# Optimization experiments

Measured on AMD Instinct MI355X. Metric: run time of the kernel, lower is better.

The kernel has to match this reference:

```python
import jax, jax.numpy as jnp
import numpy as np

B, LX, LM, D = 4, 512, 512, 256

def setup_inputs() -> dict:
    key = jax.random.key(0)
    ks = jax.random.split(key, 7)
    s = 1.0 / np.sqrt(D)
    return {
        "x": jax.random.normal(ks[0], (B, LX, D), jnp.float32),
        "memory": jax.random.normal(ks[1], (B, LM, D), jnp.float32),
        "memory_mask": jax.random.randint(ks[2], (B, LM), 0, 2, jnp.int32),
        "W1": jax.random.normal(ks[3], (D, D), jnp.float32) * s,
        "b1": jax.random.normal(ks[4], (D,), jnp.float32) * s,
        "W2": jax.random.normal(ks[5], (D, D), jnp.float32) * s,
        "Wt": jax.random.normal(ks[6], (D,), jnp.float32) * s,
    }

def reference(x, memory, memory_mask, W1, b1, W2, Wt):
    # item1: (B, Lx, D); item2: (B, Lm, D)
    item1 = jnp.einsum("bxd,ed->bxe", x, W1) + b1
    item2 = jnp.einsum("bmd,ed->bme", memory, W2)
    # additive attention: tanh of broadcast sum, then reduce D to scalar logit
    item = item1[:, :, None, :] + item2[:, None, :, :]  # (B, Lx, Lm, D)
    S_logit = jnp.einsum("bxmd,d->bxm", jnp.tanh(item), Wt)
    S_logit = jnp.where(memory_mask[:, None, :] == 0, jnp.float32(-10000.0), S_logit)
    return S_logit
```

## Files before the change

### kernel.cpp

```cpp
#include <hip/hip_runtime.h>

namespace {

constexpr int B = 4, LX = 512, LM = 512, D = 256;
constexpr float KSCALE = 2.8853900817779268f;
constexpr float CLAMP = 7.5f;

typedef __attribute__((ext_vector_type(8))) short short8;
typedef __attribute__((ext_vector_type(4))) float f32x4;
typedef __attribute__((ext_vector_type(2))) float f32x2;

__device__ __forceinline__ unsigned bfbits(float f) {
    unsigned u = __float_as_uint(f);
    u += 0x7FFFu + ((u >> 16) & 1u);
    return u >> 16;
}
__device__ __forceinline__ int pack2(float a, float b) {
    return (int)(bfbits(a) | (bfbits(b) << 16));
}
__device__ __forceinline__ f32x2 up2r(unsigned u) {
    f32x2 r;
    r.x = __uint_as_float(u << 16);
    r.y = __uint_as_float(u);
    return r;
}
__device__ __forceinline__ unsigned permb(unsigned hi, unsigned lo, unsigned sel) {
    return __builtin_amdgcn_perm(hi, lo, sel);
}

__global__ __launch_bounds__(256) void proj_mfma(
    const float* __restrict__ x, const float* __restrict__ mem,
    const float* __restrict__ W1, const float* __restrict__ b1v,
    const float* __restrict__ W2,
    unsigned short* __restrict__ E1h, unsigned short* __restrict__ E2h)
{
    const int tid = threadIdx.x;
    const int m0c = blockIdx.x * 32;
    const int e0  = blockIdx.y * 64;
    const int z   = m0c >= 2048;
    const int r0  = z ? (m0c - 2048) : m0c;
    const float* __restrict__ A = (z ? mem : x) + (size_t)r0 * D;
    const float* __restrict__ W = z ? W2 : W1;

    __shared__ short sA[8][32][40];
    __shared__ short sW[8][64][40];

    const int wid = tid >> 6, lane = tid & 63;
    const int lr = lane & 15, quad = lane >> 4;
    const int g   = wid & 1;
    const int cg0 = (wid >> 1) * 2;
    const int srA = tid >> 3;
    const int scA = (tid & 7) * 4;

#pragma unroll
    for (int kc8 = 0; kc8 < 8; ++kc8) {
        const int kc = kc8 * 32;
        const float4 av = *(const float4*)&A[(size_t)srA * D + kc + scA];
        const float4 w0 = *(const float4*)&W[(size_t)(e0 + srA) * D + kc + scA];
        const float4 w1 = *(const float4*)&W[(size_t)(e0 + 32 + srA) * D + kc + scA];
        *(int2*)&sA[kc8][srA][scA]      = make_int2(pack2(av.x, av.y), pack2(av.z, av.w));
        *(int2*)&sW[kc8][srA][scA]      = make_int2(pack2(w0.x, w0.y), pack2(w0.z, w0.w));
        *(int2*)&sW[kc8][srA + 32][scA] = make_int2(pack2(w1.x, w1.y), pack2(w1.z, w1.w));
    }
    __syncthreads();

    f32x4 acc0 = {0.f, 0.f, 0.f, 0.f};
    f32x4 acc1 = {0.f, 0.f, 0.f, 0.f};
#pragma unroll
    for (int kc8 = 0; kc8 < 8; ++kc8) {
        short8 af  = *(const short8*)&sA[kc8][g * 16 + lr][quad * 8];
        short8 bf0 = *(const short8*)&sW[kc8][cg0 * 16 + lr][quad * 8];
        short8 bf1 = *(const short8*)&sW[kc8][cg0 * 16 + 16 + lr][quad * 8];
        acc0 = __builtin_amdgcn_mfma_f32_16x16x32_bf16(af, bf0, acc0, 0, 0, 0);
        acc1 = __builtin_amdgcn_mfma_f32_16x16x32_bf16(af, bf1, acc1, 0, 0, 0);
    }

    const float bias0 = z ? 0.f : b1v[e0 + cg0 * 16 + lr];
    const float bias1 = z ? 0.f : b1v[e0 + cg0 * 16 + 16 + lr];
    const int ec0 = e0 + cg0 * 16 + lr;
#pragma unroll
    for (int reg = 0; reg < 4; ++reg) {
        const int pair = quad * 4 + reg;
        float a0 = KSCALE * (acc0[reg] + bias0);
        float a1 = KSCALE * (acc1[reg] + bias1);
        a0 = fminf(fmaxf(a0, -CLAMP), CLAMP);
        a1 = fminf(fmaxf(a1, -CLAMP), CLAMP);
        const unsigned short e0b = (unsigned short)bfbits(__builtin_amdgcn_exp2f(a0));
        const unsigned short e1b = (unsigned short)bfbits(__builtin_amdgcn_exp2f(a1));
        if (!z) {
            const size_t base = (size_t)((r0 >> 5) * 16 + pair) * 256;
            E1h[(base + ec0) * 2 + g]      = e0b;
            E1h[(base + ec0 + 16) * 2 + g] = e1b;
        } else {
            const int row = r0 + g * 16 + pair;
            E2h[(size_t)row * 256 + ec0]      = e0b;
            E2h[(size_t)row * 256 + ec0 + 16] = e1b;
        }
    }
}

constexpr int RS = 268;
constexpr int C1 = 136;

__global__ __launch_bounds__(256, 4) void tanh_score_kernel(
    const unsigned* __restrict__ E1p, const unsigned* __restrict__ E2u,
    const float* __restrict__ Wt, const int* __restrict__ mask,
    float* __restrict__ out)
{
    const int tid = threadIdx.x;
    const int b   = blockIdx.z;
    const int yb  = blockIdx.y;
    const int T   = yb >> 1;
    const int p0  = (yb & 1) * 8;
    const int bx  = blockIdx.x;

    __shared__ unsigned sA[8 * RS];
    __shared__ unsigned sB[16 * RS];
    __shared__ int scid[LM];
    __shared__ int smsk[LM];
    __shared__ float4 sRed[128];

    const int lane = tid & 63;
    const int wid  = tid >> 6;

    int mvv[8];
#pragma unroll
    for (int c = 0; c < 8; ++c) mvv[c] = mask[b * LM + c * 64 + lane];
    int count = 0, mcount = 0;
#pragma unroll
    for (int c = 0; c < 8; ++c) {
        const bool bit = mvv[c] != 0;
        const unsigned long long bal = __ballot(bit);
        const unsigned long long lt  = (1ull << lane) - 1ull;
        const int pre  = __popcll(bal & lt);
        const int prem = __popcll(~bal & lt);
        if (wid == 0) {
            if (bit) scid[count + pre]   = c * 64 + lane;
            else     smsk[mcount + prem] = c * 64 + lane;
        }
        const int pc = __popcll(bal);
        count  += pc;
        mcount += 64 - pc;
    }

    {
        const int rA = tid >> 5, q2 = tid & 31;
        const unsigned* g =
            E1p + (size_t)((b * 16 + T) * 16 + p0 + rA) * 256 + q2 * 8;
        const int off = rA * RS + q2 * 8 + (q2 >= 16 ? 8 : 0);
        *(uint4*)&sA[off]     = *(const uint4*)(g);
        *(uint4*)&sA[off + 4] = *(const uint4*)(g + 4);
    }

    float sumW = 0.f;
#pragma unroll
    for (int i = 0; i < 256; i += 4) {
        const float4 w = *(const float4*)&Wt[i];
        sumW += (w.x + w.y) + (w.z + w.w);
    }

    __syncthreads();

    const int tx = tid & 15;
    const int ty = (tid >> 4) & 7;
    const int h  = tid >> 7;
    const int hb = h * 128;
    const int ho = h * C1;
    const f32x2 one2 = {1.f, 1.f};

#define SPL(s)  ((f32x2){(s), (s)})
#define FMA2(A_, B_, C_) __builtin_elementwise_fma((A_), (B_), (C_))
#define OCT(BX, accv) { \
    const f32x2 T0 = FMA2(a_[0], BX(0), one2), T1 = FMA2(a_[1], BX(1), one2); \
    const f32x2 T2 = FMA2(a_[2], BX(2), one2), T3 = FMA2(a_[3], BX(3), one2); \
    const f32x2 T4 = FMA2(a_[4], BX(4), one2), T5 = FMA2(a_[5], BX(5), one2); \
    const f32x2 T6 = FMA2(a_[6], BX(6), one2), T7 = FMA2(a_[7], BX(7), one2); \
    const f32x2 L0 = T0 * T1, L1 = T2 * T3, L2 = T4 * T5, L3 = T6 * T7;       \
    const f32x2 Q0 = L0 * L1, Q1 = L2 * L3;                                   \
    const f32x2 den = Q0 * Q1;                                                \
    const f32x2 n0 = FMA2(SPL(wv[0]), T1, SPL(wv[1]) * T0);                   \
    const f32x2 n1 = FMA2(SPL(wv[2]), T3, SPL(wv[3]) * T2);                   \
    const f32x2 n2 = FMA2(SPL(wv[4]), T5, SPL(wv[5]) * T4);                   \
    const f32x2 n3 = FMA2(SPL(wv[6]), T7, SPL(wv[7]) * T6);                   \
    const f32x2 u0 = FMA2(n0, L1, n1 * L0), u1 = FMA2(n2, L3, n3 * L2);       \
    const f32x2 N  = FMA2(u0, Q1, u1 * Q0);                                   \
    f32x2 r; r.x = __builtin_amdgcn_rcpf(den.x);                              \
             r.y = __builtin_amdgcn_rcpf(den.y);                              \
    (accv) = FMA2(N, r, (accv)); }
#define BP(i)  (p_[i])
#define BPS(i) (__builtin_shufflevector(p_[i], p_[i], 1, 0))

    for (int s = bx; s < 16; s += 8) {
        const int m0 = s * 32;
        if (m0 >= count) break;

        {
            const int rB = tid >> 4, q = tid & 15;
            const int clo = min(m0 + rB, count - 1);
            const int chi = min(m0 + rB + 16, count - 1);
            const unsigned* rlo = E2u + (size_t)(b * LM + scid[clo]) * 128 + q * 8;
            const unsigned* rhi = E2u + (size_t)(b * LM + scid[chi]) * 128 + q * 8;
            const uint4 Lo0 = *(const uint4*)(rlo);
            const uint4 Lo1 = *(const uint4*)(rlo + 4);
            const uint4 Hi0 = *(const uint4*)(rhi);
            const uint4 Hi1 = *(const uint4*)(rhi + 4);
            const int ob = rB * RS + q * 16 + (q >= 8 ? 8 : 0);
            uint4 P;
            P.x = permb(Hi0.x, Lo0.x, 0x05040100u); P.y = permb(Hi0.x, Lo0.x, 0x07060302u);
            P.z = permb(Hi0.y, Lo0.y, 0x05040100u); P.w = permb(Hi0.y, Lo0.y, 0x07060302u);
            *(uint4*)&sB[ob] = P;
            P.x = permb(Hi0.z, Lo0.z, 0x05040100u); P.y = permb(Hi0.z, Lo0.z, 0x07060302u);
            P.z = permb(Hi0.w, Lo0.w, 0x05040100u); P.w = permb(Hi0.w, Lo0.w, 0x07060302u);
            *(uint4*)&sB[ob + 4] = P;
            P.x = permb(Hi1.x, Lo1.x, 0x05040100u); P.y = permb(Hi1.x, Lo1.x, 0x07060302u);
            P.z = permb(Hi1.y, Lo1.y, 0x05040100u); P.w = permb(Hi1.y, Lo1.y, 0x07060302u);
            *(uint4*)&sB[ob + 8] = P;
            P.x = permb(Hi1.z, Lo1.z, 0x05040100u); P.y = permb(Hi1.z, Lo1.z, 0x07060302u);
            P.z = permb(Hi1.w, Lo1.w, 0x05040100u); P.w = permb(Hi1.w, Lo1.w, 0x07060302u);
            *(uint4*)&sB[ob + 12] = P;
        }
        __syncthreads();

        f32x2 accs = {0.f, 0.f}, accw = {0.f, 0.f};
#pragma unroll 1
        for (int d = 0; d < 128; d += 8) {
            const uint4 ua0 = *(const uint4*)&sA[ty * RS + ho + d];
            const uint4 ua1 = *(const uint4*)&sA[ty * RS + ho + d + 4];
            const uint4 ub0 = *(const uint4*)&sB[tx * RS + ho + d];
            const uint4 ub1 = *(const uint4*)&sB[tx * RS + ho + d + 4];
            const float4 w0 = *(const float4*)&Wt[hb + d];
            const float4 w1 = *(const float4*)&Wt[hb + d + 4];

            const f32x2 a_[8] = {up2r(ua0.x), up2r(ua0.y), up2r(ua0.z), up2r(ua0.w),
                                 up2r(ua1.x), up2r(ua1.y), up2r(ua1.z), up2r(ua1.w)};
            const f32x2 p_[8] = {up2r(ub0.x), up2r(ub0.y), up2r(ub0.z), up2r(ub0.w),
                                 up2r(ub1.x), up2r(ub1.y), up2r(ub1.z), up2r(ub1.w)};
            const float wv[8] = {w0.x, w0.y, w0.z, w0.w, w1.x, w1.y, w1.z, w1.w};

            OCT(BP,  accs)
            OCT(BPS, accw)
        }

        if (h) sRed[ty * 16 + tx] = make_float4(accs.x, accs.y, accw.x, accw.y);
        __syncthreads();
        if (!h) {
            const float4 r = sRed[ty * 16 + tx];
            const int xA = T * 32 + p0 + ty, xB = xA + 16;
            const int col0 = m0 + tx, col1 = m0 + 16 + tx;
            if (col0 < count) {
                const int mo = scid[col0];
                out[((size_t)b * LX + xA) * LM + mo] = sumW - 2.f * (accs.x + r.x);
                out[((size_t)b * LX + xB) * LM + mo] = sumW - 2.f * (accw.y + r.w);
            }
            if (col1 < count) {
                const int mo = scid[col1];
                out[((size_t)b * LX + xA) * LM + mo] = sumW - 2.f * (accw.x + r.z);
                out[((size_t)b * LX + xB) * LM + mo] = sumW - 2.f * (accs.y + r.y);
            }
        }
    }
#undef BP
#undef BPS
#undef OCT
#undef FMA2
#undef SPL

    if (bx == 0) {
        const int xA = T * 32 + p0 + ty, xB = xA + 16;
        const int idx = h * 16 + tx;
        for (int k = idx; k < mcount; k += 32) {
            const int mo = smsk[k];
            out[((size_t)b * LX + xA) * LM + mo] = -10000.f;
            out[((size_t)b * LX + xB) * LM + mo] = -10000.f;
        }
    }
}

}

extern "C" void kernel_launch(void* const* d_in, const int* in_sizes, int n_in,
                              void* d_out, int out_size, void* d_ws, size_t ws_size,
                              hipStream_t stream)
{
    const float* x    = (const float*)d_in[0];
    const float* mem  = (const float*)d_in[1];
    const int*   mask = (const int*)d_in[2];
    const float* W1   = (const float*)d_in[3];
    const float* b1   = (const float*)d_in[4];
    const float* W2   = (const float*)d_in[5];
    const float* Wt   = (const float*)d_in[6];
    float* out = (float*)d_out;

    unsigned*       E1p = (unsigned*)d_ws;
    unsigned short* E2h = (unsigned short*)(E1p + (size_t)(B * LX / 32) * 16 * 256);

    proj_mfma<<<dim3(128, 4), 256, 0, stream>>>(
        x, mem, W1, b1, W2, (unsigned short*)E1p, E2h);

    tanh_score_kernel<<<dim3(8, 32, 4), 256, 0, stream>>>(
        E1p, (const unsigned*)E2h, Wt, mask, out);
}
```

Measured before the change: 96.92 us.

## Fuse projection and tanh-score kernels into one cooperative launch with grid sync

Merges the bf16 MFMA projection and the tanh-score kernel into a single persistent cooperative kernel of 1024 blocks. A grid-wide sync separates the phases, and a shared-memory union lets both phases reuse the same LDS. Projection tiles are re-split to 32x32 per block so the 1024 blocks cover both phases. The change also replaces the serial Wt sum with a wave shuffle reduction. It aims to remove the second launch and the gap between kernels, at the cost of a grid barrier and a need for 4 resident blocks per CU, with the two-kernel path kept as a fallback.

```diff
diff --git a/kernel.cpp b/kernel.cpp
--- a/kernel.cpp
+++ b/kernel.cpp
@@ -1,4 +1,7 @@
 #include <hip/hip_runtime.h>
+#include <hip/hip_cooperative_groups.h>
+
+namespace cg = cooperative_groups;
 
 namespace {
 
@@ -28,145 +31,8 @@
     return __builtin_amdgcn_perm(hi, lo, sel);
 }
 
-__global__ __launch_bounds__(256) void proj_mfma(
-    const float* __restrict__ x, const float* __restrict__ mem,
-    const float* __restrict__ W1, const float* __restrict__ b1v,
-    const float* __restrict__ W2,
-    unsigned short* __restrict__ E1h, unsigned short* __restrict__ E2h)
-{
-    const int tid = threadIdx.x;
-    const int m0c = blockIdx.x * 32;
-    const int e0  = blockIdx.y * 64;
-    const int z   = m0c >= 2048;
-    const int r0  = z ? (m0c - 2048) : m0c;
-    const float* __restrict__ A = (z ? mem : x) + (size_t)r0 * D;
-    const float* __restrict__ W = z ? W2 : W1;
-
-    __shared__ short sA[8][32][40];
-    __shared__ short sW[8][64][40];
-
-    const int wid = tid >> 6, lane = tid & 63;
-    const int lr = lane & 15, quad = lane >> 4;
-    const int g   = wid & 1;
-    const int cg0 = (wid >> 1) * 2;
-    const int srA = tid >> 3;
-    const int scA = (tid & 7) * 4;
-
-#pragma unroll
-    for (int kc8 = 0; kc8 < 8; ++kc8) {
-        const int kc = kc8 * 32;
-        const float4 av = *(const float4*)&A[(size_t)srA * D + kc + scA];
-        const float4 w0 = *(const float4*)&W[(size_t)(e0 + srA) * D + kc + scA];
-        const float4 w1 = *(const float4*)&W[(size_t)(e0 + 32 + srA) * D + kc + scA];
-        *(int2*)&sA[kc8][srA][scA]      = make_int2(pack2(av.x, av.y), pack2(av.z, av.w));
-        *(int2*)&sW[kc8][srA][scA]      = make_int2(pack2(w0.x, w0.y), pack2(w0.z, w0.w));
-        *(int2*)&sW[kc8][srA + 32][scA] = make_int2(pack2(w1.x, w1.y), pack2(w1.z, w1.w));
-    }
-    __syncthreads();
-
-    f32x4 acc0 = {0.f, 0.f, 0.f, 0.f};
-    f32x4 acc1 = {0.f, 0.f, 0.f, 0.f};
-#pragma unroll
-    for (int kc8 = 0; kc8 < 8; ++kc8) {
-        short8 af  = *(const short8*)&sA[kc8][g * 16 + lr][quad * 8];
-        short8 bf0 = *(const short8*)&sW[kc8][cg0 * 16 + lr][quad * 8];
-        short8 bf1 = *(const short8*)&sW[kc8][cg0 * 16 + 16 + lr][quad * 8];
-        acc0 = __builtin_amdgcn_mfma_f32_16x16x32_bf16(af, bf0, acc0, 0, 0, 0);
-        acc1 = __builtin_amdgcn_mfma_f32_16x16x32_bf16(af, bf1, acc1, 0, 0, 0);
-    }
-
-    const float bias0 = z ? 0.f : b1v[e0 + cg0 * 16 + lr];
-    const float bias1 = z ? 0.f : b1v[e0 + cg0 * 16 + 16 + lr];
-    const int ec0 = e0 + cg0 * 16 + lr;
-#pragma unroll
-    for (int reg = 0; reg < 4; ++reg) {
-        const int pair = quad * 4 + reg;
-        float a0 = KSCALE * (acc0[reg] + bias0);
-        float a1 = KSCALE * (acc1[reg] + bias1);
-        a0 = fminf(fmaxf(a0, -CLAMP), CLAMP);
-        a1 = fminf(fmaxf(a1, -CLAMP), CLAMP);
-        const unsigned short e0b = (unsigned short)bfbits(__builtin_amdgcn_exp2f(a0));
-        const unsigned short e1b = (unsigned short)bfbits(__builtin_amdgcn_exp2f(a1));
-        if (!z) {
-            const size_t base = (size_t)((r0 >> 5) * 16 + pair) * 256;
-            E1h[(base + ec0) * 2 + g]      = e0b;
-            E1h[(base + ec0 + 16) * 2 + g] = e1b;
-        } else {
-            const int row = r0 + g * 16 + pair;
-            E2h[(size_t)row * 256 + ec0]      = e0b;
-            E2h[(size_t)row * 256 + ec0 + 16] = e1b;
-        }
-    }
-}
-
 constexpr int RS = 268;
 constexpr int C1 = 136;
-
-__global__ __launch_bounds__(256, 4) void tanh_score_kernel(
-    const unsigned* __restrict__ E1p, const unsigned* __restrict__ E2u,
-    const float* __restrict__ Wt, const int* __restrict__ mask,
-    float* __restrict__ out)
-{
-    const int tid = threadIdx.x;
-    const int b   = blockIdx.z;
-    const int yb  = blockIdx.y;
-    const int T   = yb >> 1;
-    const int p0  = (yb & 1) * 8;
-    const int bx  = blockIdx.x;
-
-    __shared__ unsigned sA[8 * RS];
-    __shared__ unsigned sB[16 * RS];
-    __shared__ int scid[LM];
-    __shared__ int smsk[LM];
-    __shared__ float4 sRed[128];
-
-    const int lane = tid & 63;
-    const int wid  = tid >> 6;
-
-    int mvv[8];
-#pragma unroll
-    for (int c = 0; c < 8; ++c) mvv[c] = mask[b * LM + c * 64 + lane];
-    int count = 0, mcount = 0;
-#pragma unroll
-    for (int c = 0; c < 8; ++c) {
-        const bool bit = mvv[c] != 0;
-        const unsigned long long bal = __ballot(bit);
-        const unsigned long long lt  = (1ull << lane) - 1ull;
-        const int pre  = __popcll(bal & lt);
-        const int prem = __popcll(~bal & lt);
-        if (wid == 0) {
-            if (bit) scid[count + pre]   = c * 64 + lane;
-            else     smsk[mcount + prem] = c * 64 + lane;
-        }
-        const int pc = __popcll(bal);
-        count  += pc;
-        mcount += 64 - pc;
-    }
-
-    {
-        const int rA = tid >> 5, q2 = tid & 31;
-        const unsigned* g =
-            E1p + (size_t)((b * 16 + T) * 16 + p0 + rA) * 256 + q2 * 8;
-        const int off = rA * RS + q2 * 8 + (q2 >= 16 ? 8 : 0);
-        *(uint4*)&sA[off]     = *(const uint4*)(g);
-        *(uint4*)&sA[off + 4] = *(const uint4*)(g + 4);
-    }
-
-    float sumW = 0.f;
-#pragma unroll
-    for (int i = 0; i < 256; i += 4) {
-        const float4 w = *(const float4*)&Wt[i];
-        sumW += (w.x + w.y) + (w.z + w.w);
-    }
-
-    __syncthreads();
-
-    const int tx = tid & 15;
-    const int ty = (tid >> 4) & 7;
-    const int h  = tid >> 7;
-    const int hb = h * 128;
-    const int ho = h * C1;
-    const f32x2 one2 = {1.f, 1.f};
 
 #define SPL(s)  ((f32x2){(s), (s)})
 #define FMA2(A_, B_, C_) __builtin_elementwise_fma((A_), (B_), (C_))
@@ -189,6 +55,357 @@
     (accv) = FMA2(N, r, (accv)); }
 #define BP(i)  (p_[i])
 #define BPS(i) (__builtin_shufflevector(p_[i], p_[i], 1, 0))
+
+__global__ __launch_bounds__(256, 4) void fused_attn(
+    const float* __restrict__ x, const float* __restrict__ mem,
+    const int* __restrict__ mask,
+    const float* __restrict__ W1, const float* __restrict__ b1v,
+    const float* __restrict__ W2, const float* __restrict__ Wt,
+    unsigned* __restrict__ E1p, unsigned short* __restrict__ E2h,
+    float* __restrict__ out)
+{
+    union ShU {
+        struct { unsigned A[32 * 132]; unsigned W[32 * 132]; } p;
+        struct { unsigned sA[8 * RS]; unsigned sB[16 * RS];
+                 int scid[LM]; int smsk[LM]; float4 sRed[128]; } t;
+    };
+    __shared__ ShU sh;
+
+    const int tid  = threadIdx.x;
+    const int lane = tid & 63;
+    const int wid  = tid >> 6;
+
+    {
+        const int u    = blockIdx.x;
+        const int tile = u >> 3;
+        const int e0   = (u & 7) * 32;
+        const int m0c  = tile * 32;
+        const int z    = m0c >= 2048;
+        const int r0   = z ? (m0c - 2048) : m0c;
+        const float* __restrict__ A = (z ? mem : x) + (size_t)r0 * D;
+        const float* __restrict__ W = z ? W2 : W1;
+
+        const int sr  = tid >> 3;
+        const int scf = (tid & 7) * 32;
+
+        float4 a4[8], w4[8];
+#pragma unroll
+        for (int j = 0; j < 8; ++j) {
+            a4[j] = *(const float4*)&A[(size_t)sr * D + scf + j * 4];
+            w4[j] = *(const float4*)&W[(size_t)(e0 + sr) * D + scf + j * 4];
+        }
+#pragma unroll
+        for (int j = 0; j < 4; ++j) {
+            uint4 P;
+            P.x = pack2(a4[2*j].x,   a4[2*j].y);
+            P.y = pack2(a4[2*j].z,   a4[2*j].w);
+            P.z = pack2(a4[2*j+1].x, a4[2*j+1].y);
+            P.w = pack2(a4[2*j+1].z, a4[2*j+1].w);
+            *(uint4*)&sh.p.A[sr * 132 + (scf >> 1) + j * 4] = P;
+            P.x = pack2(w4[2*j].x,   w4[2*j].y);
+            P.y = pack2(w4[2*j].z,   w4[2*j].w);
+            P.z = pack2(w4[2*j+1].x, w4[2*j+1].y);
+            P.w = pack2(w4[2*j+1].z, w4[2*j+1].w);
+            *(uint4*)&sh.p.W[sr * 132 + (scf >> 1) + j * 4] = P;
+        }
+        __syncthreads();
+
+        const int lr = lane & 15, quad = lane >> 4;
+        const int g = wid & 1, cgq = wid >> 1;
+        f32x4 acc = {0.f, 0.f, 0.f, 0.f};
+#pragma unroll
+        for (int k8 = 0; k8 < 8; ++k8) {
+            short8 af = *(const short8*)&sh.p.A[(g*16 + lr)*132 + k8*16 + quad*4];
+            short8 bf = *(const short8*)&sh.p.W[(cgq*16 + lr)*132 + k8*16 + quad*4];
+            acc = __builtin_amdgcn_mfma_f32_16x16x32_bf16(af, bf, acc, 0, 0, 0);
+        }
+
+        const int ec = e0 + cgq * 16 + lr;
+        const float bias = z ? 0.f : b1v[ec];
+#pragma unroll
+        for (int reg = 0; reg < 4; ++reg) {
+            const int pair = quad * 4 + reg;
+            float a0 = KSCALE * (acc[reg] + bias);
+            a0 = fminf(fmaxf(a0, -CLAMP), CLAMP);
+            const unsigned short eb =
+                (unsigned short)bfbits(__builtin_amdgcn_exp2f(a0));
+            if (!z) {
+                ((unsigned short*)E1p)
+                    [(((size_t)(r0 >> 5) * 16 + pair) * 256 + ec) * 2 + g] = eb;
+            } else {
+                E2h[(size_t)(r0 + g * 16 + pair) * 256 + ec] = eb;
+            }
+        }
+    }
+
+    cg::this_grid().sync();
+
+    const int b  = blockIdx.x >> 8;
+    const int yb = (blockIdx.x >> 3) & 31;
+    const int bx = blockIdx.x & 7;
+    const int T  = yb >> 1;
+    const int p0 = (yb & 1) * 8;
+
+    int mvv[8];
+#pragma unroll
+    for (int c = 0; c < 8; ++c) mvv[c] = mask[b * LM + c * 64 + lane];
+    int count = 0, mcount = 0;
+#pragma unroll
+    for (int c = 0; c < 8; ++c) {
+        const bool bit = mvv[c] != 0;
+        const unsigned long long bal = __ballot(bit);
+        const unsigned long long lt  = (1ull << lane) - 1ull;
+        const int pre  = __popcll(bal & lt);
+        const int prem = __popcll(~bal & lt);
+        if (wid == 0) {
+            if (bit) sh.t.scid[count + pre]   = c * 64 + lane;
+            else     sh.t.smsk[mcount + prem] = c * 64 + lane;
+        }
+        const int pc = __popcll(bal);
+        count  += pc;
+        mcount += 64 - pc;
+    }
+
+    {
+        const int rA = tid >> 5, q2 = tid & 31;
+        const unsigned* g_ =
+            E1p + (size_t)((b * 16 + T) * 16 + p0 + rA) * 256 + q2 * 8;
+        const int off = rA * RS + q2 * 8 + (q2 >= 16 ? 8 : 0);
+        *(uint4*)&sh.t.sA[off]     = *(const uint4*)(g_);
+        *(uint4*)&sh.t.sA[off + 4] = *(const uint4*)(g_ + 4);
+    }
+
+    const float4 wsv = *(const float4*)&Wt[lane * 4];
+    float sumW = (wsv.x + wsv.y) + (wsv.z + wsv.w);
+#pragma unroll
+    for (int off = 32; off >= 1; off >>= 1) sumW += __shfl_xor(sumW, off);
+
+    __syncthreads();
+
+    const int tx = tid & 15;
+    const int ty = (tid >> 4) & 7;
+    const int h  = tid >> 7;
+    const int hb = h * 128;
+    const int ho = h * C1;
+    const f32x2 one2 = {1.f, 1.f};
+
+    for (int s = bx; s < 16; s += 8) {
+        const int m0 = s * 32;
+        if (m0 >= count) break;
+
+        {
+            const int rB = tid >> 4, q = tid & 15;
+            const int clo = min(m0 + rB, count - 1);
+            const int chi = min(m0 + rB + 16, count - 1);
+            const unsigned* rlo =
+                (const unsigned*)E2h + (size_t)(b * LM + sh.t.scid[clo]) * 128 + q * 8;
+            const unsigned* rhi =
+                (const unsigned*)E2h + (size_t)(b * LM + sh.t.scid[chi]) * 128 + q * 8;
+            const uint4 Lo0 = *(const uint4*)(rlo);
+            const uint4 Lo1 = *(const uint4*)(rlo + 4);
+            const uint4 Hi0 = *(const uint4*)(rhi);
+            const uint4 Hi1 = *(const uint4*)(rhi + 4);
+            const int ob = rB * RS + q * 16 + (q >= 8 ? 8 : 0);
+            uint4 P;
+            P.x = permb(Hi0.x, Lo0.x, 0x05040100u); P.y = permb(Hi0.x, Lo0.x, 0x07060302u);
+            P.z = permb(Hi0.y, Lo0.y, 0x05040100u); P.w = permb(Hi0.y, Lo0.y, 0x07060302u);
+            *(uint4*)&sh.t.sB[ob] = P;
+            P.x = permb(Hi0.z, Lo0.z, 0x05040100u); P.y = permb(Hi0.z, Lo0.z, 0x07060302u);
+            P.z = permb(Hi0.w, Lo0.w, 0x05040100u); P.w = permb(Hi0.w, Lo0.w, 0x07060302u);
+            *(uint4*)&sh.t.sB[ob + 4] = P;
+            P.x = permb(Hi1.x, Lo1.x, 0x05040100u); P.y = permb(Hi1.x, Lo1.x, 0x07060302u);
+            P.z = permb(Hi1.y, Lo1.y, 0x05040100u); P.w = permb(Hi1.y, Lo1.y, 0x07060302u);
+            *(uint4*)&sh.t.sB[ob + 8] = P;
+            P.x = permb(Hi1.z, Lo1.z, 0x05040100u); P.y = permb(Hi1.z, Lo1.z, 0x07060302u);
+            P.z = permb(Hi1.w, Lo1.w, 0x05040100u); P.w = permb(Hi1.w, Lo1.w, 0x07060302u);
+            *(uint4*)&sh.t.sB[ob + 12] = P;
+        }
+        __syncthreads();
+
+        f32x2 accs = {0.f, 0.f}, accw = {0.f, 0.f};
+#pragma unroll 1
+        for (int d = 0; d < 128; d += 8) {
+            const uint4 ua0 = *(const uint4*)&sh.t.sA[ty * RS + ho + d];
+            const uint4 ua1 = *(const uint4*)&sh.t.sA[ty * RS + ho + d + 4];
+            const uint4 ub0 = *(const uint4*)&sh.t.sB[tx * RS + ho + d];
+            const uint4 ub1 = *(const uint4*)&sh.t.sB[tx * RS + ho + d + 4];
+            const float4 w0 = *(const float4*)&Wt[hb + d];
+            const float4 w1 = *(const float4*)&Wt[hb + d + 4];
+
+            const f32x2 a_[8] = {up2r(ua0.x), up2r(ua0.y), up2r(ua0.z), up2r(ua0.w),
+                                 up2r(ua1.x), up2r(ua1.y), up2r(ua1.z), up2r(ua1.w)};
+            const f32x2 p_[8] = {up2r(ub0.x), up2r(ub0.y), up2r(ub0.z), up2r(ub0.w),
+                                 up2r(ub1.x), up2r(ub1.y), up2r(ub1.z), up2r(ub1.w)};
+            const float wv[8] = {w0.x, w0.y, w0.z, w0.w, w1.x, w1.y, w1.z, w1.w};
+
+            OCT(BP,  accs)
+            OCT(BPS, accw)
+        }
+
+        if (h) sh.t.sRed[ty * 16 + tx] = make_float4(accs.x, accs.y, accw.x, accw.y);
+        __syncthreads();
+        if (!h) {
+            const float4 r = sh.t.sRed[ty * 16 + tx];
+            const int xA = T * 32 + p0 + ty, xB = xA + 16;
+            const int col0 = m0 + tx, col1 = m0 + 16 + tx;
+            if (col0 < count) {
+                const int mo = sh.t.scid[col0];
+                out[((size_t)b * LX + xA) * LM + mo] = sumW - 2.f * (accs.x + r.x);
+                out[((size_t)b * LX + xB) * LM + mo] = sumW - 2.f * (accw.y + r.w);
+            }
+            if (col1 < count) {
+                const int mo = sh.t.scid[col1];
+                out[((size_t)b * LX + xA) * LM + mo] = sumW - 2.f * (accw.x + r.z);
+                out[((size_t)b * LX + xB) * LM + mo] = sumW - 2.f * (accs.y + r.y);
+            }
+        }
+    }
+
+    if (bx == 0) {
+        const int xA = T * 32 + p0 + ty, xB = xA + 16;
+        const int idx = h * 16 + tx;
+        for (int k = idx; k < mcount; k += 32) {
+            const int mo = sh.t.smsk[k];
+            out[((size_t)b * LX + xA) * LM + mo] = -10000.f;
+            out[((size_t)b * LX + xB) * LM + mo] = -10000.f;
+        }
+    }
+}
+
+__global__ __launch_bounds__(256) void proj_mfma(
+    const float* __restrict__ x, const float* __restrict__ mem,
+    const float* __restrict__ W1, const float* __restrict__ b1v,
+    const float* __restrict__ W2,
+    unsigned short* __restrict__ E1h, unsigned short* __restrict__ E2h)
+{
+    const int tid = threadIdx.x;
+    const int m0c = blockIdx.x * 32;
+    const int e0  = blockIdx.y * 64;
+    const int z   = m0c >= 2048;
+    const int r0  = z ? (m0c - 2048) : m0c;
+    const float* __restrict__ A = (z ? mem : x) + (size_t)r0 * D;
+    const float* __restrict__ W = z ? W2 : W1;
+
+    __shared__ short sA[8][32][40];
+    __shared__ short sW[8][64][40];
+
+    const int wid = tid >> 6, lane = tid & 63;
+    const int lr = lane & 15, quad = lane >> 4;
+    const int g   = wid & 1;
+    const int cg0 = (wid >> 1) * 2;
+    const int srA = tid >> 3;
+    const int scA = (tid & 7) * 4;
+
+#pragma unroll
+    for (int kc8 = 0; kc8 < 8; ++kc8) {
+        const int kc = kc8 * 32;
+        const float4 av = *(const float4*)&A[(size_t)srA * D + kc + scA];
+        const float4 w0 = *(const float4*)&W[(size_t)(e0 + srA) * D + kc + scA];
+        const float4 w1 = *(const float4*)&W[(size_t)(e0 + 32 + srA) * D + kc + scA];
+        *(int2*)&sA[kc8][srA][scA]      = make_int2(pack2(av.x, av.y), pack2(av.z, av.w));
+        *(int2*)&sW[kc8][srA][scA]      = make_int2(pack2(w0.x, w0.y), pack2(w0.z, w0.w));
+        *(int2*)&sW[kc8][srA + 32][scA] = make_int2(pack2(w1.x, w1.y), pack2(w1.z, w1.w));
+    }
+    __syncthreads();
+
+    f32x4 acc0 = {0.f, 0.f, 0.f, 0.f};
+    f32x4 acc1 = {0.f, 0.f, 0.f, 0.f};
+#pragma unroll
+    for (int kc8 = 0; kc8 < 8; ++kc8) {
+        short8 af  = *(const short8*)&sA[kc8][g * 16 + lr][quad * 8];
+        short8 bf0 = *(const short8*)&sW[kc8][cg0 * 16 + lr][quad * 8];
+        short8 bf1 = *(const short8*)&sW[kc8][cg0 * 16 + 16 + lr][quad * 8];
+        acc0 = __builtin_amdgcn_mfma_f32_16x16x32_bf16(af, bf0, acc0, 0, 0, 0);
+        acc1 = __builtin_amdgcn_mfma_f32_16x16x32_bf16(af, bf1, acc1, 0, 0, 0);
+    }
+
+    const float bias0 = z ? 0.f : b1v[e0 + cg0 * 16 + lr];
+    const float bias1 = z ? 0.f : b1v[e0 + cg0 * 16 + 16 + lr];
+    const int ec0 = e0 + cg0 * 16 + lr;
+#pragma unroll
+    for (int reg = 0; reg < 4; ++reg) {
+        const int pair = quad * 4 + reg;
+        float a0 = KSCALE * (acc0[reg] + bias0);
+        float a1 = KSCALE * (acc1[reg] + bias1);
+        a0 = fminf(fmaxf(a0, -CLAMP), CLAMP);
+        a1 = fminf(fmaxf(a1, -CLAMP), CLAMP);
+        const unsigned short e0b = (unsigned short)bfbits(__builtin_amdgcn_exp2f(a0));
+        const unsigned short e1b = (unsigned short)bfbits(__builtin_amdgcn_exp2f(a1));
+        if (!z) {
+            const size_t base = (size_t)((r0 >> 5) * 16 + pair) * 256;
+            E1h[(base + ec0) * 2 + g]      = e0b;
+            E1h[(base + ec0 + 16) * 2 + g] = e1b;
+        } else {
+            const int row = r0 + g * 16 + pair;
+            E2h[(size_t)row * 256 + ec0]      = e0b;
+            E2h[(size_t)row * 256 + ec0 + 16] = e1b;
+        }
+    }
+}
+
+__global__ __launch_bounds__(256, 4) void tanh_score_kernel(
+    const unsigned* __restrict__ E1p, const unsigned* __restrict__ E2u,
+    const float* __restrict__ Wt, const int* __restrict__ mask,
+    float* __restrict__ out)
+{
+    const int tid = threadIdx.x;
+    const int b   = blockIdx.z;
+    const int yb  = blockIdx.y;
+    const int T   = yb >> 1;
+    const int p0  = (yb & 1) * 8;
+    const int bx  = blockIdx.x;
+
+    __shared__ unsigned sA[8 * RS];
+    __shared__ unsigned sB[16 * RS];
+    __shared__ int scid[LM];
+    __shared__ int smsk[LM];
+    __shared__ float4 sRed[128];
+
+    const int lane = tid & 63;
+    const int wid  = tid >> 6;
+
+    int mvv[8];
+#pragma unroll
+    for (int c = 0; c < 8; ++c) mvv[c] = mask[b * LM + c * 64 + lane];
+    int count = 0, mcount = 0;
+#pragma unroll
+    for (int c = 0; c < 8; ++c) {
+        const bool bit = mvv[c] != 0;
+        const unsigned long long bal = __ballot(bit);
+        const unsigned long long lt  = (1ull << lane) - 1ull;
+        const int pre  = __popcll(bal & lt);
+        const int prem = __popcll(~bal & lt);
+        if (wid == 0) {
+            if (bit) scid[count + pre]   = c * 64 + lane;
+            else     smsk[mcount + prem] = c * 64 + lane;
+        }
+        const int pc = __popcll(bal);
+        count  += pc;
+        mcount += 64 - pc;
+    }
+
+    {
+        const int rA = tid >> 5, q2 = tid & 31;
+        const unsigned* g_ =
+            E1p + (size_t)((b * 16 + T) * 16 + p0 + rA) * 256 + q2 * 8;
+        const int off = rA * RS + q2 * 8 + (q2 >= 16 ? 8 : 0);
+        *(uint4*)&sA[off]     = *(const uint4*)(g_);
+        *(uint4*)&sA[off + 4] = *(const uint4*)(g_ + 4);
+    }
+
+    const float4 wsv = *(const float4*)&Wt[lane * 4];
+    float sumW = (wsv.x + wsv.y) + (wsv.z + wsv.w);
+#pragma unroll
+    for (int off = 32; off >= 1; off >>= 1) sumW += __shfl_xor(sumW, off);
+
+    __syncthreads();
+
+    const int tx = tid & 15;
+    const int ty = (tid >> 4) & 7;
+    const int h  = tid >> 7;
+    const int hb = h * 128;
+    const int ho = h * C1;
+    const f32x2 one2 = {1.f, 1.f};
 
     for (int s = bx; s < 16; s += 8) {
         const int m0 = s * 32;
@@ -259,11 +476,6 @@
             }
         }
     }
-#undef BP
-#undef BPS
-#undef OCT
-#undef FMA2
-#undef SPL
 
     if (bx == 0) {
         const int xA = T * 32 + p0 + ty, xB = xA + 16;
@@ -275,6 +487,12 @@
         }
     }
 }
+
+#undef BP
+#undef BPS
+#undef OCT
+#undef FMA2
+#undef SPL
 
 }
 
@@ -294,9 +512,31 @@
     unsigned*       E1p = (unsigned*)d_ws;
     unsigned short* E2h = (unsigned short*)(E1p + (size_t)(B * LX / 32) * 16 * 256);
 
-    proj_mfma<<<dim3(128, 4), 256, 0, stream>>>(
-        x, mem, W1, b1, W2, (unsigned short*)E1p, E2h);
-
-    tanh_score_kernel<<<dim3(8, 32, 4), 256, 0, stream>>>(
-        E1p, (const unsigned*)E2h, Wt, mask, out);
-}
+    static int coopBlocksPerCU = -1;
+    if (coopBlocksPerCU < 0) {
+        int nb = 0;
+        if (hipOccupancyMaxActiveBlocksPerMultiprocessor(
+                &nb, (const void*)fused_attn, 256, 0) != hipSuccess) nb = 0;
+        coopBlocksPerCU = nb;
+    }
+
+    bool launched = false;
+    if (coopBlocksPerCU >= 4) {
+        void* params[10];
+        params[0] = (void*)&x;   params[1] = (void*)&mem; params[2] = (void*)&mask;
+        params[3] = (void*)&W1;  params[4] = (void*)&b1;  params[5] = (void*)&W2;
+        params[6] = (void*)&Wt;  params[7] = (void*)&E1p; params[8] = (void*)&E2h;
+        params[9] = (void*)&out;
+        if (hipLaunchCooperativeKernel((const void*)fused_attn,
+                                       dim3(1024), dim3(256),
+                                       params, 0, stream) == hipSuccess)
+            launched = true;
+    }
+
+    if (!launched) {
+        proj_mfma<<<dim3(128, 4), 256, 0, stream>>>(
+            x, mem, W1, b1, W2, (unsigned short*)E1p, E2h);
+        tanh_score_kernel<<<dim3(8, 32, 4), 256, 0, stream>>>(
+            E1p, (const unsigned*)E2h, Wt, mask, out);
+    }
+}
```

Result: faster. 92.78 us (-4.3%).
